# Kernel tuning notes

Measured on AMD Instinct MI355X. Metric: run time of the kernel, lower is better.

Reference implementation:

```python
import jax, jax.numpy as jnp
import numpy as np

B, F, BLOCK = 8192, 3072, 3


def _det3(a):
    # analytic determinant of (..., 3, 3)
    return (a[..., 0, 0] * (a[..., 1, 1] * a[..., 2, 2] - a[..., 1, 2] * a[..., 2, 1])
            - a[..., 0, 1] * (a[..., 1, 0] * a[..., 2, 2] - a[..., 1, 2] * a[..., 2, 0])
            + a[..., 0, 2] * (a[..., 1, 0] * a[..., 2, 1] - a[..., 1, 1] * a[..., 2, 0]))


def setup_inputs() -> dict:
    key = jax.random.key(0)
    k1, k2 = jax.random.split(key)
    x = jax.random.normal(k1, (B, F), dtype=jnp.float32)
    # w must be strictly inside the unit sphere per block: normalize to radius 0.5
    g = jax.random.normal(k2, (B, F), dtype=jnp.float32).reshape(B, F // BLOCK, BLOCK)
    g = 0.5 * g / jnp.linalg.norm(g, axis=-1, keepdims=True)
    return {"x": x, "w": g.reshape(B, F), "blocks": BLOCK}


def _moebius(x, w, block):
    batch, nfeat = x.shape
    nb = nfeat // block
    xb = x.reshape(batch, nb, block)   # (B, nb, d)
    wb = w.reshape(batch, nb, block)
    x_norm = jnp.sqrt(jnp.sum(xb * xb, axis=-1, keepdims=True))        # (B, nb, 1)
    xn = xb / x_norm                                                   # normalized x
    xpw = xn + wb
    wns = jnp.sum(wb * wb, axis=-1, keepdims=True)                     # |w|^2
    xwns = jnp.sum(xpw * xpw, axis=-1, keepdims=True)                  # |xn+w|^2
    yn = (1.0 - wns) / xwns * xpw + wb                                 # y_normalized
    y = x_norm * yn

    # block Jacobian dy/dx, shape (B, nb, d, d)
    eye = jnp.eye(block, dtype=x.dtype)
    xn4 = x_norm[..., None]            # (B, nb, 1, 1)
    dxn_dx = (eye - xb[..., :, None] * xb[..., None, :] / (xn4 * xn4)) / xn4
    g = jnp.einsum('bnij,bnj->bni', dxn_dx, xpw)
    J = (2.0 / xwns[..., None]) * (xpw[..., :, None] * g[..., None, :])
    J = xn4 * (1.0 - wns[..., None]) / xwns[..., None] * (dxn_dx - J)
    J = J + yn[..., :, None] * xn[..., None, :]

    log_det_J = jnp.sum(jnp.log(jnp.abs(_det3(J))), axis=1)            # (B,)
    return y.reshape(batch, nfeat), log_det_J


def reference(x, w, blocks):
    return _moebius(x, w, blocks)
```

## Files before the change

kernel.cpp:

```cpp
#include <hip/hip_runtime.h>
#include <math.h>

#define BATCH 8192
#define FEAT  3072
#define TPB   256


__global__ __launch_bounds__(TPB, 8)
void moebius_kernel(const float* __restrict__ x,
                    const float* __restrict__ w,
                    float* __restrict__ out) {
    __shared__ float swred[TPB / 64];

    const int row = blockIdx.x;
    const int tid = threadIdx.x;
    const size_t base = (size_t)row * FEAT + 12 * tid;

    const float4* __restrict__ x4 = (const float4*)(x + base);
    const float4* __restrict__ w4 = (const float4*)(w + base);

    const float4 xa = x4[0], xb = x4[1], xc = x4[2];
    const float4 wa = w4[0], wb = w4[1], wc = w4[2];

    const float X[12] = {xa.x, xa.y, xa.z, xa.w, xb.x, xb.y, xb.z, xb.w,
                         xc.x, xc.y, xc.z, xc.w};
    const float W[12] = {wa.x, wa.y, wa.z, wa.w, wb.x, wb.y, wb.z, wb.w,
                         wc.x, wc.y, wc.z, wc.w};
    float Y[12];

    float lsum = 0.0f;

    #pragma unroll
    for (int j = 0; j < 4; ++j) {
        const float x0 = X[3 * j], x1 = X[3 * j + 1], x2 = X[3 * j + 2];
        const float w0 = W[3 * j], w1 = W[3 * j + 1], w2 = W[3 * j + 2];

        const float r2   = fmaxf(x0 * x0 + x1 * x1 + x2 * x2, 1e-30f);
        const float invr = __builtin_amdgcn_rsqf(r2);
        const float r    = r2 * invr;

        const float p0 = x0 * invr + w0;
        const float p1 = x1 * invr + w1;
        const float p2 = x2 * invr + w2;

        const float wns  = w0 * w0 + w1 * w1 + w2 * w2;
        const float xwns = fmaxf(p0 * p0 + p1 * p1 + p2 * p2, 1e-30f);
        const float c    = (1.0f - wns) * __builtin_amdgcn_rcpf(xwns);

        Y[3 * j]     = r * (c * p0 + w0);
        Y[3 * j + 1] = r * (c * p1 + w1);
        Y[3 * j + 2] = r * (c * p2 + w2);

        lsum += __builtin_amdgcn_logf(c);
    }

    float4* __restrict__ y4 = (float4*)(out + base);
    y4[0] = make_float4(Y[0], Y[1], Y[2],  Y[3]);
    y4[1] = make_float4(Y[4], Y[5], Y[6],  Y[7]);
    y4[2] = make_float4(Y[8], Y[9], Y[10], Y[11]);

    #pragma unroll
    for (int off = 32; off > 0; off >>= 1) {
        lsum += __shfl_down(lsum, off, 64);
    }
    const int lane = tid & 63;
    const int wave = tid >> 6;
    if (lane == 0) swred[wave] = lsum;
    __syncthreads();
    if (tid == 0) {
        const float tot = (swred[0] + swred[1] + swred[2] + swred[3]) * 1.3862943611f;
        out[(size_t)BATCH * FEAT + row] = tot;
    }
}

extern "C" void kernel_launch(void* const* d_in, const int* in_sizes, int n_in,
                              void* d_out, int out_size, void* d_ws, size_t ws_size,
                              hipStream_t stream) {
    const float* x = (const float*)d_in[0];
    const float* w = (const float*)d_in[1];
    float* out = (float*)d_out;

    moebius_kernel<<<BATCH, TPB, 0, stream>>>(x, w, out);
}
```

Baseline: 240.0 us.

## Process four rows per workgroup with double-buffered register prefetch

Each workgroup now handles four rows instead of one, and the next row's x and w loads are issued into a second register buffer before the current row is computed. This is meant to keep more memory requests in flight per thread and to spread the launch and reduction overhead over more work. In exchange it cuts the grid by a factor of four and raises register use, with the occupancy hint lowered from 8 to 6, which may limit latency hiding on a memory-bound kernel.

```diff
diff --git a/kernel.cpp b/kernel.cpp
--- a/kernel.cpp
+++ b/kernel.cpp
@@ -4,72 +4,89 @@
 #define BATCH 8192
 #define FEAT  3072
 #define TPB   256
+#define ROWS  4
+#define NWG   (BATCH / ROWS)
+#define RS4   (FEAT / 4)
 
 
-__global__ __launch_bounds__(TPB, 8)
+__global__ __launch_bounds__(TPB, 6)
 void moebius_kernel(const float* __restrict__ x,
                     const float* __restrict__ w,
                     float* __restrict__ out) {
-    __shared__ float swred[TPB / 64];
+    __shared__ float swred[TPB / 64][ROWS];
 
-    const int row = blockIdx.x;
-    const int tid = threadIdx.x;
-    const size_t base = (size_t)row * FEAT + 12 * tid;
+    const int tid  = threadIdx.x;
+    const int lane = tid & 63;
+    const int wave = tid >> 6;
+    const size_t base = (size_t)blockIdx.x * ROWS * FEAT + 12 * tid;
 
     const float4* __restrict__ x4 = (const float4*)(x + base);
     const float4* __restrict__ w4 = (const float4*)(w + base);
+    float4* __restrict__ y4       = (float4*)(out + base);
 
-    const float4 xa = x4[0], xb = x4[1], xc = x4[2];
-    const float4 wa = w4[0], wb = w4[1], wc = w4[2];
-
-    const float X[12] = {xa.x, xa.y, xa.z, xa.w, xb.x, xb.y, xb.z, xb.w,
-                         xc.x, xc.y, xc.z, xc.w};
-    const float W[12] = {wa.x, wa.y, wa.z, wa.w, wb.x, wb.y, wb.z, wb.w,
-                         wc.x, wc.y, wc.z, wc.w};
-    float Y[12];
-
-    float lsum = 0.0f;
+    float4 bx[2][3], bw[2][3];
+    bx[0][0] = x4[0]; bx[0][1] = x4[1]; bx[0][2] = x4[2];
+    bw[0][0] = w4[0]; bw[0][1] = w4[1]; bw[0][2] = w4[2];
 
     #pragma unroll
-    for (int j = 0; j < 4; ++j) {
-        const float x0 = X[3 * j], x1 = X[3 * j + 1], x2 = X[3 * j + 2];
-        const float w0 = W[3 * j], w1 = W[3 * j + 1], w2 = W[3 * j + 2];
+    for (int i = 0; i < ROWS; ++i) {
+        const int cur = i & 1;
+        if (i + 1 < ROWS) {
+            const int nxt = cur ^ 1;
+            const int o = (i + 1) * RS4;
+            bx[nxt][0] = x4[o + 0]; bx[nxt][1] = x4[o + 1]; bx[nxt][2] = x4[o + 2];
+            bw[nxt][0] = w4[o + 0]; bw[nxt][1] = w4[o + 1]; bw[nxt][2] = w4[o + 2];
+        }
 
-        const float r2   = fmaxf(x0 * x0 + x1 * x1 + x2 * x2, 1e-30f);
-        const float invr = __builtin_amdgcn_rsqf(r2);
-        const float r    = r2 * invr;
+        const float4 xa = bx[cur][0], xb = bx[cur][1], xc = bx[cur][2];
+        const float4 wa = bw[cur][0], wb = bw[cur][1], wc = bw[cur][2];
+        const float X[12] = {xa.x, xa.y, xa.z, xa.w, xb.x, xb.y, xb.z, xb.w,
+                             xc.x, xc.y, xc.z, xc.w};
+        const float W[12] = {wa.x, wa.y, wa.z, wa.w, wb.x, wb.y, wb.z, wb.w,
+                             wc.x, wc.y, wc.z, wc.w};
+        float Y[12];
+        float lsum = 0.0f;
 
-        const float p0 = x0 * invr + w0;
-        const float p1 = x1 * invr + w1;
-        const float p2 = x2 * invr + w2;
+        #pragma unroll
+        for (int j = 0; j < 4; ++j) {
+            const float x0 = X[3 * j], x1 = X[3 * j + 1], x2 = X[3 * j + 2];
+            const float w0 = W[3 * j], w1 = W[3 * j + 1], w2 = W[3 * j + 2];
 
-        const float wns  = w0 * w0 + w1 * w1 + w2 * w2;
-        const float xwns = fmaxf(p0 * p0 + p1 * p1 + p2 * p2, 1e-30f);
-        const float c    = (1.0f - wns) * __builtin_amdgcn_rcpf(xwns);
+            const float r2   = fmaxf(x0 * x0 + x1 * x1 + x2 * x2, 1e-30f);
+            const float invr = __builtin_amdgcn_rsqf(r2);
+            const float r    = r2 * invr;
 
-        Y[3 * j]     = r * (c * p0 + w0);
-        Y[3 * j + 1] = r * (c * p1 + w1);
-        Y[3 * j + 2] = r * (c * p2 + w2);
+            const float p0 = x0 * invr + w0;
+            const float p1 = x1 * invr + w1;
+            const float p2 = x2 * invr + w2;
 
-        lsum += __builtin_amdgcn_logf(c);
+            const float wns  = w0 * w0 + w1 * w1 + w2 * w2;
+            const float xwns = fmaxf(p0 * p0 + p1 * p1 + p2 * p2, 1e-30f);
+            const float cc   = (1.0f - wns) * __builtin_amdgcn_rcpf(xwns);
+
+            Y[3 * j]     = r * (cc * p0 + w0);
+            Y[3 * j + 1] = r * (cc * p1 + w1);
+            Y[3 * j + 2] = r * (cc * p2 + w2);
+
+            lsum += __builtin_amdgcn_logf(cc);
+        }
+
+        y4[i * RS4 + 0] = make_float4(Y[0], Y[1], Y[2],  Y[3]);
+        y4[i * RS4 + 1] = make_float4(Y[4], Y[5], Y[6],  Y[7]);
+        y4[i * RS4 + 2] = make_float4(Y[8], Y[9], Y[10], Y[11]);
+
+        #pragma unroll
+        for (int off = 32; off > 0; off >>= 1) {
+            lsum += __shfl_down(lsum, off, 64);
+        }
+        if (lane == 0) swred[wave][i] = lsum;
     }
 
-    float4* __restrict__ y4 = (float4*)(out + base);
-    y4[0] = make_float4(Y[0], Y[1], Y[2],  Y[3]);
-    y4[1] = make_float4(Y[4], Y[5], Y[6],  Y[7]);
-    y4[2] = make_float4(Y[8], Y[9], Y[10], Y[11]);
-
-    #pragma unroll
-    for (int off = 32; off > 0; off >>= 1) {
-        lsum += __shfl_down(lsum, off, 64);
-    }
-    const int lane = tid & 63;
-    const int wave = tid >> 6;
-    if (lane == 0) swred[wave] = lsum;
     __syncthreads();
-    if (tid == 0) {
-        const float tot = (swred[0] + swred[1] + swred[2] + swred[3]) * 1.3862943611f;
-        out[(size_t)BATCH * FEAT + row] = tot;
+    if (tid < ROWS) {
+        const float tot = (swred[0][tid] + swred[1][tid] +
+                           swred[2][tid] + swred[3][tid]) * 1.3862943611f;
+        out[(size_t)BATCH * FEAT + (size_t)blockIdx.x * ROWS + tid] = tot;
     }
 }
 
@@ -80,5 +97,5 @@
     const float* w = (const float*)d_in[1];
     float* out = (float*)d_out;
 
-    moebius_kernel<<<BATCH, TPB, 0, stream>>>(x, w, out);
+    moebius_kernel<<<NWG, TPB, 0, stream>>>(x, w, out);
 }
```

After: 252.5 us. 5.2% more time.
